# Optimization experiments

Hardware: AMD Instinct MI355X
Metric: run time of the kernel (lower is better)

## Reference

```python
import jax, jax.numpy as jnp
import numpy as np
import math

B, L, HD, H = 4, 1024, 512, 8
D = HD // H  # 64 per-head dim


def setup_inputs() -> dict:
    key = jax.random.key(0)
    ks = jax.random.split(key, 9)
    query = jax.random.normal(ks[0], (B, L, HD), jnp.float32)
    key_ = jax.random.normal(ks[1], (B, L, HD), jnp.float32)
    value = jax.random.normal(ks[2], (B, L, HD), jnp.float32)
    kernel = jax.random.normal(ks[3], (B * H, L, L), jnp.float32) * 0.1
    # sparse-ish boolean mask; low density so no row is fully masked
    attn_mask = jax.random.bernoulli(ks[4], 0.05, (B * H, L, L))
    in_proj_weight = jax.random.normal(ks[5], (3 * HD, HD), jnp.float32) * 0.02
    in_proj_bias = jnp.zeros((3 * HD,), jnp.float32)
    out_w = jax.random.normal(ks[6], (HD, HD), jnp.float32) * 0.02
    out_b = jnp.zeros((HD,), jnp.float32)
    return dict(query=query, key_=key_, value=value, attn_mask=attn_mask,
                key_padding_mask=0, kernel=kernel,
                in_proj_weight=in_proj_weight, in_proj_bias=in_proj_bias,
                out_w=out_w, out_b=out_b)


def _split_heads(x):
    # [B, L, HD] -> [B*H, L, D]
    b, l, _ = x.shape
    return x.reshape(b, l, H, D).transpose(0, 2, 1, 3).reshape(b * H, l, D)


def _merge_heads(x):
    # [B*H, L, D] -> [B, L, HD]
    bh, l, d = x.shape
    b = bh // H
    return x.reshape(b, H, l, d).transpose(0, 2, 1, 3).reshape(b, l, H * d)


def reference(query, key_, value, attn_mask, key_padding_mask, kernel,
              in_proj_weight, in_proj_bias, out_w, out_b):
    # key_padding_mask is falsy (None-equivalent) -> attn_mask unchanged
    wq, wk, wv = in_proj_weight[:HD], in_proj_weight[HD:2 * HD], in_proj_weight[2 * HD:]
    bq, bk, bv = in_proj_bias[:HD], in_proj_bias[HD:2 * HD], in_proj_bias[2 * HD:]
    q = _split_heads(query @ wq.T + bq)   # [B*H, L, D]
    k = _split_heads(key_ @ wk.T + bk)
    v = _split_heads(value @ wv.T + bv)
    scale = 1.0 / math.sqrt(D)
    scores = jnp.einsum('bqd,bkd->bqk', q, k) * scale  # [B*H, Lq, Lk]
    scores = scores + kernel.transpose(0, 2, 1)        # additive kernel bias
    scores = jnp.where(attn_mask, -jnp.inf, scores)    # masked_fill
    attn = jax.nn.softmax(scores, axis=-1)
    out = jnp.einsum('bqk,bkd->bqd', attn, v)          # [B*H, Lq, D]
    out = _merge_heads(out)                            # [B, Lq, HD]
    return out @ out_w.T + out_b
```

## Files before the change

kernel.cpp:

```cpp
#include <hip/hip_runtime.h>
#include <hip/hip_bf16.h>
#include <cstdint>
#include <cstddef>

typedef _Float16 half8 __attribute__((ext_vector_type(8)));
typedef _Float16 half4 __attribute__((ext_vector_type(4)));
typedef float f32x4 __attribute__((ext_vector_type(4)));

#define NB 4
#define NL 1024
#define NHD 512
#define NH 8
#define ND 64
#define NBH 32

#define MFMA16(a, b, c) __builtin_amdgcn_mfma_f32_16x16x32_f16((a), (b), (c), 0, 0, 0)

__global__ __launch_bounds__(256) void prep_kernel(
    const float* __restrict__ kern, const void* __restrict__ mask,
    _Float16* __restrict__ kf16, unsigned* __restrict__ mb)
{
    const int tid = threadIdx.x;
    if (blockIdx.x < 2048) {
        const size_t n8 = (size_t)NBH * NL * NL / 8;
        const size_t stride = 2048 * 256;
        for (size_t u = (size_t)blockIdx.x * 256 + tid; u < n8; u += stride) {
            const float* s = kern + u * 8;
            f32x4 a = *(const f32x4*)s;
            f32x4 b = *(const f32x4*)(s + 4);
            half8 h;
#pragma unroll
            for (int j = 0; j < 4; ++j) { h[j] = (_Float16)a[j]; h[4 + j] = (_Float16)b[j]; }
            *(half8*)(kf16 + u * 8) = h;
        }
    } else {
        __shared__ int s_byte;
        const int blk = blockIdx.x - 2048;
        for (int it = 0; it < 4; ++it) {
            const int t = (blk * 4 + it) * 256 + tid;
            __syncthreads();
            if (tid == 0) s_byte = 0;
            __syncthreads();

            const uint4* p = (const uint4*)((const unsigned char*)mask + (size_t)t * 32);
            uint4 a = p[0], b = p[1];
            unsigned src[8] = {a.x, a.y, a.z, a.w, b.x, b.y, b.z, b.w};
            int bad = 0;
#pragma unroll
            for (int j = 0; j < 8; ++j)
                if (src[j] != 0u && src[j] != 1u && src[j] != 0x3F800000u) bad = 1;
            if (bad) atomicOr(&s_byte, 1);
            __syncthreads();

            unsigned wv = 0;
            if (s_byte) {
#pragma unroll
                for (int j = 0; j < 8; ++j) {
                    unsigned u = src[j];
                    wv |= ((u & 0x000000FFu) ? 1u : 0u) << (4 * j + 0);
                    wv |= ((u & 0x0000FF00u) ? 1u : 0u) << (4 * j + 1);
                    wv |= ((u & 0x00FF0000u) ? 1u : 0u) << (4 * j + 2);
                    wv |= ((u & 0xFF000000u) ? 1u : 0u) << (4 * j + 3);
                }
            } else {
                const uint4* q = (const uint4*)((const unsigned*)mask + (size_t)t * 32);
#pragma unroll
                for (int j = 0; j < 8; ++j) {
                    uint4 v = q[j];
                    wv |= (v.x ? 1u : 0u) << (4 * j + 0);
                    wv |= (v.y ? 1u : 0u) << (4 * j + 1);
                    wv |= (v.z ? 1u : 0u) << (4 * j + 2);
                    wv |= (v.w ? 1u : 0u) << (4 * j + 3);
                }
            }
            mb[t] = wv;
        }
    }
}

__global__ __launch_bounds__(256) void qkv_gemm_kernel(
    const float* __restrict__ qin, const float* __restrict__ kin, const float* __restrict__ vin,
    const float* __restrict__ w, const float* __restrict__ bias,
    _Float16* __restrict__ qb, _Float16* __restrict__ kb, _Float16* __restrict__ vtb)
{
    const int mtile = blockIdx.x, ntile = blockIdx.y, proj = blockIdx.z;
    const float* A = proj == 0 ? qin : (proj == 1 ? kin : vin);
    const float* W = w + (size_t)proj * NHD * NHD;

    __shared__ __align__(16) _Float16 a_lds[128][72];
    __shared__ __align__(16) _Float16 b_lds[64][72];

    const int tid = threadIdx.x;
    const int wave = tid >> 6, lane = tid & 63, quad = lane >> 4, c = lane & 15;
    const int wm = wave >> 1, wn = wave & 1;

    f32x4 acc[4][2] = {};

    const int arow = tid >> 1, acol = (tid & 1) * 32;
    const int brow = tid >> 2, bcol = (tid & 3) * 16;
    const float* pa = &A[(size_t)(mtile * 128 + arow) * NHD + acol];
    const float* pb = &W[(size_t)(ntile * 64 + brow) * NHD + bcol];

    f32x4 ar[8], br[4];
#pragma unroll
    for (int j = 0; j < 8; ++j) ar[j] = *(const f32x4*)(pa + j * 4);
#pragma unroll
    for (int j = 0; j < 4; ++j) br[j] = *(const f32x4*)(pb + j * 4);

    for (int k0 = 0; k0 < NHD; k0 += 64) {
        half8 ah[4], bh_[2];
#pragma unroll
        for (int t = 0; t < 4; ++t)
#pragma unroll
            for (int j = 0; j < 4; ++j) {
                ah[t][j] = (_Float16)ar[2 * t][j];
                ah[t][4 + j] = (_Float16)ar[2 * t + 1][j];
            }
#pragma unroll
        for (int t = 0; t < 2; ++t)
#pragma unroll
            for (int j = 0; j < 4; ++j) {
                bh_[t][j] = (_Float16)br[2 * t][j];
                bh_[t][4 + j] = (_Float16)br[2 * t + 1][j];
            }
        __syncthreads();
#pragma unroll
        for (int t = 0; t < 4; ++t) *(half8*)&a_lds[arow][acol + t * 8] = ah[t];
#pragma unroll
        for (int t = 0; t < 2; ++t) *(half8*)&b_lds[brow][bcol + t * 8] = bh_[t];
        if (k0 < NHD - 64) {
            const float* na = pa + k0 + 64;
            const float* nb = pb + k0 + 64;
#pragma unroll
            for (int j = 0; j < 8; ++j) ar[j] = *(const f32x4*)(na + j * 4);
#pragma unroll
            for (int j = 0; j < 4; ++j) br[j] = *(const f32x4*)(nb + j * 4);
        }
        __syncthreads();

#pragma unroll
        for (int kk = 0; kk < 2; ++kk) {
            half8 af[4], bf[2];
#pragma unroll
            for (int ms = 0; ms < 4; ++ms)
                af[ms] = *(const half8*)&a_lds[wm * 64 + ms * 16 + c][kk * 32 + quad * 8];
#pragma unroll
            for (int ns = 0; ns < 2; ++ns)
                bf[ns] = *(const half8*)&b_lds[wn * 32 + ns * 16 + c][kk * 32 + quad * 8];
#pragma unroll
            for (int ms = 0; ms < 4; ++ms)
#pragma unroll
                for (int ns = 0; ns < 2; ++ns)
                    acc[ms][ns] = MFMA16(af[ms], bf[ns], acc[ms][ns]);
        }
    }

#pragma unroll
    for (int ms = 0; ms < 4; ++ms)
#pragma unroll
    for (int ns = 0; ns < 2; ++ns) {
        const int Cc = ntile * 64 + wn * 32 + ns * 16 + c;
        const float bv = bias[proj * NHD + Cc];
        const int h = Cc >> 6, d = Cc & 63;
#pragma unroll
        for (int r = 0; r < 4; ++r) {
            const int R = mtile * 128 + wm * 64 + ms * 16 + quad * 4 + r;
            const int b = R >> 10, l = R & 1023;
            const int bh = b * NH + h;
            float val = acc[ms][ns][r] + bv;
            if (proj == 0) {
                qb[((size_t)(bh * NL + l)) * ND + d] = (_Float16)(val * 0.125f);
            } else if (proj == 1) {
                kb[((size_t)(bh * NL + l)) * ND + d] = (_Float16)val;
            } else {
                vtb[((size_t)(bh * ND + d)) * NL + l] = (_Float16)val;
            }
        }
    }
}

__global__ __launch_bounds__(256) void attn_kernel(
    const _Float16* __restrict__ qb, const _Float16* __restrict__ kb, const _Float16* __restrict__ vtb,
    const _Float16* __restrict__ kf16, const unsigned* __restrict__ mb,
    _Float16* __restrict__ pO, float* __restrict__ pm, float* __restrict__ pl)
{
    const int qt = blockIdx.x, bh = blockIdx.y, half = blockIdx.z;
    const int tid = threadIdx.x, wave = tid >> 6, lane = tid & 63, quad = lane >> 4, c = lane & 15;
    const int q_base = qt * 64 + wave * 16;
    const int kt0 = half * 8;

    __shared__ __align__(16) _Float16 k_lds[64][72];
    __shared__ __align__(16) _Float16 vt_lds[64][72];
    __shared__ __align__(16) _Float16 p_lds[64][72];
    __shared__ unsigned mask_lds[64][2];

    half8 aq0 = *(const half8*)&qb[((size_t)(bh * NL) + q_base + c) * ND + quad * 8];
    half8 aq1 = *(const half8*)&qb[((size_t)(bh * NL) + q_base + c) * ND + 32 + quad * 8];

    f32x4 O[4] = {};
    float m_i[4] = {-1e30f, -1e30f, -1e30f, -1e30f};
    float l_i[4] = {0.f, 0.f, 0.f, 0.f};

    const int sr = tid >> 2, sc = (tid & 3) * 16;

    half8 kr0, kr1, vr0, vr1;
    unsigned mr = 0;
    half4 bias_h[4];

    const _Float16* bias_base = kf16 + (size_t)bh * NL * NL + (size_t)(qt * 64 + wave * 16 + quad * 4);

    {
        const _Float16* pk = &kb[((size_t)(bh * NL) + kt0 * 64 + sr) * ND + sc];
        kr0 = *(const half8*)pk; kr1 = *(const half8*)(pk + 8);
        const _Float16* pv = &vtb[((size_t)(bh * ND) + sr) * NL + kt0 * 64 + sc];
        vr0 = *(const half8*)pv; vr1 = *(const half8*)(pv + 8);
        if (tid < 128) mr = mb[((size_t)bh * NL + qt * 64 + (tid >> 1)) * 32 + kt0 * 2 + (tid & 1)];
#pragma unroll
        for (int ns = 0; ns < 4; ++ns)
            bias_h[ns] = *(const half4*)(bias_base + (size_t)(kt0 * 64 + ns * 16 + c) * NL);
    }

    for (int kt = 0; kt < 8; ++kt) {
        __syncthreads();
        *(half8*)&k_lds[sr][sc] = kr0;  *(half8*)&k_lds[sr][sc + 8] = kr1;
        *(half8*)&vt_lds[sr][sc] = vr0; *(half8*)&vt_lds[sr][sc + 8] = vr1;
        if (tid < 128) mask_lds[tid >> 1][tid & 1] = mr;
        __syncthreads();

        if (kt < 7) {
            const int ktg = kt0 + kt + 1;
            const _Float16* pk = &kb[((size_t)(bh * NL) + ktg * 64 + sr) * ND + sc];
            kr0 = *(const half8*)pk; kr1 = *(const half8*)(pk + 8);
            const _Float16* pv = &vtb[((size_t)(bh * ND) + sr) * NL + ktg * 64 + sc];
            vr0 = *(const half8*)pv; vr1 = *(const half8*)(pv + 8);
            if (tid < 128) mr = mb[((size_t)bh * NL + qt * 64 + (tid >> 1)) * 32 + ktg * 2 + (tid & 1)];
        }

        f32x4 S[4];
#pragma unroll
        for (int ns = 0; ns < 4; ++ns) {
            f32x4 a = {};
            half8 bk0 = *(const half8*)&k_lds[ns * 16 + c][quad * 8];
            half8 bk1 = *(const half8*)&k_lds[ns * 16 + c][32 + quad * 8];
            a = MFMA16(aq0, bk0, a);
            a = MFMA16(aq1, bk1, a);
            S[ns] = a;
        }

        unsigned mw0[4], mw1[4];
#pragma unroll
        for (int r = 0; r < 4; ++r) {
            const int row = wave * 16 + quad * 4 + r;
            uint2 mm = *(const uint2*)&mask_lds[row][0];
            mw0[r] = mm.x; mw1[r] = mm.y;
        }

#pragma unroll
        for (int ns = 0; ns < 4; ++ns) {
            const int bit = ((ns & 1) << 4) + c;
#pragma unroll
            for (int r = 0; r < 4; ++r) {
                unsigned w = (ns < 2) ? mw0[r] : mw1[r];
                bool mk = (w >> bit) & 1u;
                S[ns][r] = mk ? -1e30f : (S[ns][r] + (float)bias_h[ns][r]);
            }
        }

        if (kt < 7) {
            const int ktg = kt0 + kt + 1;
#pragma unroll
            for (int ns = 0; ns < 4; ++ns)
                bias_h[ns] = *(const half4*)(bias_base + (size_t)(ktg * 64 + ns * 16 + c) * NL);
        }

        float pmax[4], al[4];
#pragma unroll
        for (int r = 0; r < 4; ++r) {
            float t = fmaxf(fmaxf(S[0][r], S[1][r]), fmaxf(S[2][r], S[3][r]));
            t = fmaxf(t, __shfl_xor(t, 1));
            t = fmaxf(t, __shfl_xor(t, 2));
            t = fmaxf(t, __shfl_xor(t, 4));
            t = fmaxf(t, __shfl_xor(t, 8));
            float mn = fmaxf(m_i[r], t);
            al[r] = __expf(m_i[r] - mn);
            m_i[r] = mn;
            pmax[r] = mn;
        }
        float rs[4] = {0.f, 0.f, 0.f, 0.f};
#pragma unroll
        for (int ns = 0; ns < 4; ++ns)
#pragma unroll
            for (int r = 0; r < 4; ++r) {
                float p = __expf(S[ns][r] - pmax[r]);
                S[ns][r] = p;
                rs[r] += p;
            }
#pragma unroll
        for (int r = 0; r < 4; ++r) {
            float t = rs[r];
            t += __shfl_xor(t, 1);
            t += __shfl_xor(t, 2);
            t += __shfl_xor(t, 4);
            t += __shfl_xor(t, 8);
            l_i[r] = l_i[r] * al[r] + t;
        }
#pragma unroll
        for (int ds = 0; ds < 4; ++ds)
#pragma unroll
            for (int r = 0; r < 4; ++r)
                O[ds][r] *= al[r];

#pragma unroll
        for (int ns = 0; ns < 4; ++ns)
#pragma unroll
            for (int r = 0; r < 4; ++r)
                p_lds[wave * 16 + quad * 4 + r][ns * 16 + c] = (_Float16)S[ns][r];
        __asm__ volatile("s_waitcnt lgkmcnt(0)" ::: "memory");

#pragma unroll
        for (int ks = 0; ks < 2; ++ks) {
            half8 ap = *(const half8*)&p_lds[wave * 16 + c][ks * 32 + quad * 8];
#pragma unroll
            for (int ds = 0; ds < 4; ++ds) {
                half8 bv = *(const half8*)&vt_lds[ds * 16 + c][ks * 32 + quad * 8];
                O[ds] = MFMA16(ap, bv, O[ds]);
            }
        }
    }

    const int ub = (bh * 16 + qt) * 2 + half;
    _Float16* pOb = pO + (size_t)ub * 4096;
#pragma unroll
    for (int ds = 0; ds < 4; ++ds)
#pragma unroll
        for (int r = 0; r < 4; ++r)
            pOb[(wave * 16 + quad * 4 + r) * 64 + ds * 16 + c] = (_Float16)O[ds][r];
    if (c == 0) {
#pragma unroll
        for (int r = 0; r < 4; ++r) {
            const int row = wave * 16 + quad * 4 + r;
            pm[(size_t)ub * 64 + row] = m_i[r];
            pl[(size_t)ub * 64 + row] = l_i[r];
        }
    }
}

__global__ __launch_bounds__(256) void out_gemm_kernel(
    const _Float16* __restrict__ pO, const float* __restrict__ pm, const float* __restrict__ pl,
    const float* __restrict__ w, const float* __restrict__ bias,
    float* __restrict__ out)
{
    const int mtile = blockIdx.x, ntile = blockIdx.y;
    const int bb = mtile >> 4, qt = mtile & 15;
    __shared__ __align__(16) _Float16 a_lds[64][72];
    __shared__ __align__(16) _Float16 b_lds[64][72];
    const int tid = threadIdx.x, wave = tid >> 6, lane = tid & 63, quad = lane >> 4, c = lane & 15;
    const int wm = wave >> 1, wn = wave & 1;
    f32x4 acc[2][2] = {};

    const int sr = tid >> 2, sc = (tid & 3) * 16;

    half8 p0a, p0b, p1a, p1b;
    f32x4 br[4];
    float m0, l0, m1, l1;

    auto fetch = [&](int k0) {
        const int h = k0 >> 6;
        const int u0 = ((bb * 8 + h) * 16 + qt) * 2;
        const _Float16* q0 = pO + (size_t)u0 * 4096 + sr * 64 + sc;
        p0a = *(const half8*)q0; p0b = *(const half8*)(q0 + 8);
        const _Float16* q1 = q0 + 4096;
        p1a = *(const half8*)q1; p1b = *(const half8*)(q1 + 8);
        m0 = pm[(size_t)u0 * 64 + sr]; l0 = pl[(size_t)u0 * 64 + sr];
        m1 = pm[(size_t)(u0 + 1) * 64 + sr]; l1 = pl[(size_t)(u0 + 1) * 64 + sr];
        const float* pb = &w[(size_t)(ntile * 64 + sr) * NHD + k0 + sc];
#pragma unroll
        for (int j = 0; j < 4; ++j) br[j] = *(const f32x4*)(pb + j * 4);
    };

    fetch(0);
    for (int k0 = 0; k0 < NHD; k0 += 64) {
        const float mx = fmaxf(m0, m1);
        const float e0 = __expf(m0 - mx), e1 = __expf(m1 - mx);
        const float linv = 1.0f / (l0 * e0 + l1 * e1);
        const float s0 = e0 * linv, s1 = e1 * linv;
        half8 ah0, ah1, bh0, bh1;
#pragma unroll
        for (int j = 0; j < 8; ++j) {
            ah0[j] = (_Float16)((float)p0a[j] * s0 + (float)p1a[j] * s1);
            ah1[j] = (_Float16)((float)p0b[j] * s0 + (float)p1b[j] * s1);
        }
#pragma unroll
        for (int j = 0; j < 4; ++j) {
            bh0[j] = (_Float16)br[0][j]; bh0[4 + j] = (_Float16)br[1][j];
            bh1[j] = (_Float16)br[2][j]; bh1[4 + j] = (_Float16)br[3][j];
        }
        __syncthreads();
        *(half8*)&a_lds[sr][sc] = ah0; *(half8*)&a_lds[sr][sc + 8] = ah1;
        *(half8*)&b_lds[sr][sc] = bh0; *(half8*)&b_lds[sr][sc + 8] = bh1;
        if (k0 < NHD - 64) fetch(k0 + 64);
        __syncthreads();

#pragma unroll
        for (int kk = 0; kk < 2; ++kk) {
            half8 af0 = *(const half8*)&a_lds[wm * 32 + c][kk * 32 + quad * 8];
            half8 af1 = *(const half8*)&a_lds[wm * 32 + 16 + c][kk * 32 + quad * 8];
            half8 bf0 = *(const half8*)&b_lds[wn * 32 + c][kk * 32 + quad * 8];
            half8 bf1 = *(const half8*)&b_lds[wn * 32 + 16 + c][kk * 32 + quad * 8];
            acc[0][0] = MFMA16(af0, bf0, acc[0][0]);
            acc[0][1] = MFMA16(af0, bf1, acc[0][1]);
            acc[1][0] = MFMA16(af1, bf0, acc[1][0]);
            acc[1][1] = MFMA16(af1, bf1, acc[1][1]);
        }
    }

#pragma unroll
    for (int ms = 0; ms < 2; ++ms)
#pragma unroll
    for (int ns = 0; ns < 2; ++ns) {
        const int Cc = ntile * 64 + wn * 32 + ns * 16 + c;
        const float bv = bias[Cc];
#pragma unroll
        for (int r = 0; r < 4; ++r) {
            const int R = mtile * 64 + wm * 32 + ms * 16 + quad * 4 + r;
            out[(size_t)R * NHD + Cc] = acc[ms][ns][r] + bv;
        }
    }
}

extern "C" void kernel_launch(void* const* d_in, const int* in_sizes, int n_in,
                              void* d_out, int out_size, void* d_ws, size_t ws_size,
                              hipStream_t stream)
{
    const float* query = (const float*)d_in[0];
    const float* key_  = (const float*)d_in[1];
    const float* value = (const float*)d_in[2];
    const void*  mask  = d_in[3];
    const float* kern  = (const float*)d_in[5];
    const float* ipw   = (const float*)d_in[6];
    const float* ipb   = (const float*)d_in[7];
    const float* outw  = (const float*)d_in[8];
    const float* outb  = (const float*)d_in[9];

    char* ws = (char*)d_ws;
    _Float16* qb  = (_Float16*)(ws);
    _Float16* kb  = (_Float16*)(ws + (4ull << 20));
    _Float16* vtb = (_Float16*)(ws + (8ull << 20));
    _Float16* pO  = (_Float16*)(ws + (16ull << 20));
    float* pm     = (float*)(ws + (32ull << 20));
    float* pl     = (float*)(ws + (33ull << 20));
    unsigned* mb  = (unsigned*)(ws + (40ull << 20));
    _Float16* kf16= (_Float16*)(ws + (48ull << 20));

    prep_kernel<<<3072, 256, 0, stream>>>(kern, mask, kf16, mb);
    qkv_gemm_kernel<<<dim3(32, 8, 3), 256, 0, stream>>>(query, key_, value, ipw, ipb, qb, kb, vtb);
    attn_kernel<<<dim3(16, 32, 2), 256, 0, stream>>>(qb, kb, vtb, kf16, mb, pO, pm, pl);
    out_gemm_kernel<<<dim3(64, 8), 256, 0, stream>>>(pO, pm, pl, outw, outb, (float*)d_out);
}
```

Before: 409.6 us.

## Read fp32 bias directly in attention, process 256 query rows per block

Removes the separate pass that converted the 128 MB fp32 bias kernel to fp16 and instead loads fp32 bias directly inside the attention kernel as f32x4 vectors of four consecutive query rows. Each block now handles 256 query rows (four 64-row sub-tiles, with Q staged in LDS), so bias reads cover wider contiguous spans and K/V tiles are reused across more queries. This cuts a full read-plus-write of the bias tensor, but raises register pressure (four sets of O, m and l accumulators plus 16 f32x4 bias loads) and leaves only 256 blocks, which may reduce occupancy.

```diff
diff --git a/kernel.cpp b/kernel.cpp
--- a/kernel.cpp
+++ b/kernel.cpp
@@ -16,65 +16,49 @@
 
 #define MFMA16(a, b, c) __builtin_amdgcn_mfma_f32_16x16x32_f16((a), (b), (c), 0, 0, 0)
 
-__global__ __launch_bounds__(256) void prep_kernel(
-    const float* __restrict__ kern, const void* __restrict__ mask,
-    _Float16* __restrict__ kf16, unsigned* __restrict__ mb)
+__global__ __launch_bounds__(256) void mask_kernel(
+    const void* __restrict__ mask, unsigned* __restrict__ mb)
 {
+    __shared__ int s_byte;
     const int tid = threadIdx.x;
-    if (blockIdx.x < 2048) {
-        const size_t n8 = (size_t)NBH * NL * NL / 8;
-        const size_t stride = 2048 * 256;
-        for (size_t u = (size_t)blockIdx.x * 256 + tid; u < n8; u += stride) {
-            const float* s = kern + u * 8;
-            f32x4 a = *(const f32x4*)s;
-            f32x4 b = *(const f32x4*)(s + 4);
-            half8 h;
-#pragma unroll
-            for (int j = 0; j < 4; ++j) { h[j] = (_Float16)a[j]; h[4 + j] = (_Float16)b[j]; }
-            *(half8*)(kf16 + u * 8) = h;
-        }
-    } else {
-        __shared__ int s_byte;
-        const int blk = blockIdx.x - 2048;
-        for (int it = 0; it < 4; ++it) {
-            const int t = (blk * 4 + it) * 256 + tid;
-            __syncthreads();
-            if (tid == 0) s_byte = 0;
-            __syncthreads();
-
-            const uint4* p = (const uint4*)((const unsigned char*)mask + (size_t)t * 32);
-            uint4 a = p[0], b = p[1];
-            unsigned src[8] = {a.x, a.y, a.z, a.w, b.x, b.y, b.z, b.w};
-            int bad = 0;
-#pragma unroll
-            for (int j = 0; j < 8; ++j)
-                if (src[j] != 0u && src[j] != 1u && src[j] != 0x3F800000u) bad = 1;
-            if (bad) atomicOr(&s_byte, 1);
-            __syncthreads();
-
-            unsigned wv = 0;
-            if (s_byte) {
-#pragma unroll
-                for (int j = 0; j < 8; ++j) {
-                    unsigned u = src[j];
-                    wv |= ((u & 0x000000FFu) ? 1u : 0u) << (4 * j + 0);
-                    wv |= ((u & 0x0000FF00u) ? 1u : 0u) << (4 * j + 1);
-                    wv |= ((u & 0x00FF0000u) ? 1u : 0u) << (4 * j + 2);
-                    wv |= ((u & 0xFF000000u) ? 1u : 0u) << (4 * j + 3);
-                }
-            } else {
-                const uint4* q = (const uint4*)((const unsigned*)mask + (size_t)t * 32);
-#pragma unroll
-                for (int j = 0; j < 8; ++j) {
-                    uint4 v = q[j];
-                    wv |= (v.x ? 1u : 0u) << (4 * j + 0);
-                    wv |= (v.y ? 1u : 0u) << (4 * j + 1);
-                    wv |= (v.z ? 1u : 0u) << (4 * j + 2);
-                    wv |= (v.w ? 1u : 0u) << (4 * j + 3);
-                }
-            }
-            mb[t] = wv;
-        }
+    for (int it = 0; it < 4; ++it) {
+        const int t = (blockIdx.x * 4 + it) * 256 + tid;
+        __syncthreads();
+        if (tid == 0) s_byte = 0;
+        __syncthreads();
+
+        const uint4* p = (const uint4*)((const unsigned char*)mask + (size_t)t * 32);
+        uint4 a = p[0], b = p[1];
+        unsigned src[8] = {a.x, a.y, a.z, a.w, b.x, b.y, b.z, b.w};
+        int bad = 0;
+#pragma unroll
+        for (int j = 0; j < 8; ++j)
+            if (src[j] != 0u && src[j] != 1u && src[j] != 0x3F800000u) bad = 1;
+        if (bad) atomicOr(&s_byte, 1);
+        __syncthreads();
+
+        unsigned wv = 0;
+        if (s_byte) {
+#pragma unroll
+            for (int j = 0; j < 8; ++j) {
+                unsigned u = src[j];
+                wv |= ((u & 0x000000FFu) ? 1u : 0u) << (4 * j + 0);
+                wv |= ((u & 0x0000FF00u) ? 1u : 0u) << (4 * j + 1);
+                wv |= ((u & 0x00FF0000u) ? 1u : 0u) << (4 * j + 2);
+                wv |= ((u & 0xFF000000u) ? 1u : 0u) << (4 * j + 3);
+            }
+        } else {
+            const uint4* q = (const uint4*)((const unsigned*)mask + (size_t)t * 32);
+#pragma unroll
+            for (int j = 0; j < 8; ++j) {
+                uint4 v = q[j];
+                wv |= (v.x ? 1u : 0u) << (4 * j + 0);
+                wv |= (v.y ? 1u : 0u) << (4 * j + 1);
+                wv |= (v.z ? 1u : 0u) << (4 * j + 2);
+                wv |= (v.w ? 1u : 0u) << (4 * j + 3);
+            }
+        }
+        mb[t] = wv;
     }
 }
 
@@ -181,50 +165,56 @@
 
 __global__ __launch_bounds__(256) void attn_kernel(
     const _Float16* __restrict__ qb, const _Float16* __restrict__ kb, const _Float16* __restrict__ vtb,
-    const _Float16* __restrict__ kf16, const unsigned* __restrict__ mb,
+    const float* __restrict__ kern, const unsigned* __restrict__ mb,
     _Float16* __restrict__ pO, float* __restrict__ pm, float* __restrict__ pl)
 {
-    const int qt = blockIdx.x, bh = blockIdx.y, half = blockIdx.z;
+    const int qt4 = blockIdx.x, bh = blockIdx.y, half = blockIdx.z;
     const int tid = threadIdx.x, wave = tid >> 6, lane = tid & 63, quad = lane >> 4, c = lane & 15;
-    const int q_base = qt * 64 + wave * 16;
     const int kt0 = half * 8;
+    const int q0 = qt4 * 256;
 
     __shared__ __align__(16) _Float16 k_lds[64][72];
     __shared__ __align__(16) _Float16 vt_lds[64][72];
     __shared__ __align__(16) _Float16 p_lds[64][72];
-    __shared__ unsigned mask_lds[64][2];
-
-    half8 aq0 = *(const half8*)&qb[((size_t)(bh * NL) + q_base + c) * ND + quad * 8];
-    half8 aq1 = *(const half8*)&qb[((size_t)(bh * NL) + q_base + c) * ND + 32 + quad * 8];
-
-    f32x4 O[4] = {};
-    float m_i[4] = {-1e30f, -1e30f, -1e30f, -1e30f};
-    float l_i[4] = {0.f, 0.f, 0.f, 0.f};
+    __shared__ __align__(16) _Float16 q_lds[256][72];
+    __shared__ __align__(8) unsigned mask_lds[256][2];
 
     const int sr = tid >> 2, sc = (tid & 3) * 16;
 
+#pragma unroll
+    for (int seg = 0; seg < 4; ++seg) {
+        const int row = seg * 64 + sr;
+        const _Float16* src = &qb[((size_t)(bh * NL) + q0 + row) * ND + sc];
+        half8 a = *(const half8*)src, b = *(const half8*)(src + 8);
+        *(half8*)&q_lds[row][sc] = a;
+        *(half8*)&q_lds[row][sc + 8] = b;
+    }
+
+    f32x4 O[4][4] = {};
+    float m_i[4][4], l_i[4][4];
+#pragma unroll
+    for (int s = 0; s < 4; ++s)
+#pragma unroll
+        for (int r = 0; r < 4; ++r) { m_i[s][r] = -1e30f; l_i[s][r] = 0.f; }
+
     half8 kr0, kr1, vr0, vr1;
-    unsigned mr = 0;
-    half4 bias_h[4];
-
-    const _Float16* bias_base = kf16 + (size_t)bh * NL * NL + (size_t)(qt * 64 + wave * 16 + quad * 4);
+    uint2 mrow;
+
+    const float* bias_base = kern + (size_t)bh * NL * NL + (size_t)(q0 + wave * 16 + quad * 4);
 
     {
         const _Float16* pk = &kb[((size_t)(bh * NL) + kt0 * 64 + sr) * ND + sc];
         kr0 = *(const half8*)pk; kr1 = *(const half8*)(pk + 8);
         const _Float16* pv = &vtb[((size_t)(bh * ND) + sr) * NL + kt0 * 64 + sc];
         vr0 = *(const half8*)pv; vr1 = *(const half8*)(pv + 8);
-        if (tid < 128) mr = mb[((size_t)bh * NL + qt * 64 + (tid >> 1)) * 32 + kt0 * 2 + (tid & 1)];
-#pragma unroll
-        for (int ns = 0; ns < 4; ++ns)
-            bias_h[ns] = *(const half4*)(bias_base + (size_t)(kt0 * 64 + ns * 16 + c) * NL);
+        mrow = *(const uint2*)&mb[((size_t)bh * NL + q0 + tid) * 32 + kt0 * 2];
     }
 
     for (int kt = 0; kt < 8; ++kt) {
         __syncthreads();
         *(half8*)&k_lds[sr][sc] = kr0;  *(half8*)&k_lds[sr][sc + 8] = kr1;
         *(half8*)&vt_lds[sr][sc] = vr0; *(half8*)&vt_lds[sr][sc + 8] = vr1;
-        if (tid < 128) mask_lds[tid >> 1][tid & 1] = mr;
+        *(uint2*)&mask_lds[tid][0] = mrow;
         __syncthreads();
 
         if (kt < 7) {
@@ -233,114 +223,124 @@
             kr0 = *(const half8*)pk; kr1 = *(const half8*)(pk + 8);
             const _Float16* pv = &vtb[((size_t)(bh * ND) + sr) * NL + ktg * 64 + sc];
             vr0 = *(const half8*)pv; vr1 = *(const half8*)(pv + 8);
-            if (tid < 128) mr = mb[((size_t)bh * NL + qt * 64 + (tid >> 1)) * 32 + ktg * 2 + (tid & 1)];
-        }
-
-        f32x4 S[4];
-#pragma unroll
-        for (int ns = 0; ns < 4; ++ns) {
-            f32x4 a = {};
-            half8 bk0 = *(const half8*)&k_lds[ns * 16 + c][quad * 8];
-            half8 bk1 = *(const half8*)&k_lds[ns * 16 + c][32 + quad * 8];
-            a = MFMA16(aq0, bk0, a);
-            a = MFMA16(aq1, bk1, a);
-            S[ns] = a;
-        }
-
-        unsigned mw0[4], mw1[4];
-#pragma unroll
-        for (int r = 0; r < 4; ++r) {
-            const int row = wave * 16 + quad * 4 + r;
-            uint2 mm = *(const uint2*)&mask_lds[row][0];
-            mw0[r] = mm.x; mw1[r] = mm.y;
-        }
-
-#pragma unroll
-        for (int ns = 0; ns < 4; ++ns) {
-            const int bit = ((ns & 1) << 4) + c;
+            mrow = *(const uint2*)&mb[((size_t)bh * NL + q0 + tid) * 32 + ktg * 2];
+        }
+
+        const int kta = kt0 + kt;
+        f32x4 bias_r[4][4];
+#pragma unroll
+        for (int s = 0; s < 4; ++s)
+#pragma unroll
+            for (int ns = 0; ns < 4; ++ns)
+                bias_r[s][ns] = *(const f32x4*)(bias_base + (size_t)(kta * 64 + ns * 16 + c) * NL + s * 64);
+
+#pragma unroll
+        for (int s = 0; s < 4; ++s) {
+            half8 aq0 = *(const half8*)&q_lds[s * 64 + wave * 16 + c][quad * 8];
+            half8 aq1 = *(const half8*)&q_lds[s * 64 + wave * 16 + c][32 + quad * 8];
+
+            f32x4 S[4];
+#pragma unroll
+            for (int ns = 0; ns < 4; ++ns) {
+                f32x4 a = {};
+                half8 bk0 = *(const half8*)&k_lds[ns * 16 + c][quad * 8];
+                half8 bk1 = *(const half8*)&k_lds[ns * 16 + c][32 + quad * 8];
+                a = MFMA16(aq0, bk0, a);
+                a = MFMA16(aq1, bk1, a);
+                S[ns] = a;
+            }
+
+            unsigned mw0[4], mw1[4];
 #pragma unroll
             for (int r = 0; r < 4; ++r) {
-                unsigned w = (ns < 2) ? mw0[r] : mw1[r];
-                bool mk = (w >> bit) & 1u;
-                S[ns][r] = mk ? -1e30f : (S[ns][r] + (float)bias_h[ns][r]);
-            }
-        }
-
-        if (kt < 7) {
-            const int ktg = kt0 + kt + 1;
+                const int row = s * 64 + wave * 16 + quad * 4 + r;
+                uint2 mm = *(const uint2*)&mask_lds[row][0];
+                mw0[r] = mm.x; mw1[r] = mm.y;
+            }
+
+#pragma unroll
+            for (int ns = 0; ns < 4; ++ns) {
+                const int bit = ((ns & 1) << 4) + c;
+#pragma unroll
+                for (int r = 0; r < 4; ++r) {
+                    unsigned w = (ns < 2) ? mw0[r] : mw1[r];
+                    bool mk = (w >> bit) & 1u;
+                    S[ns][r] = mk ? -1e30f : (S[ns][r] + bias_r[s][ns][r]);
+                }
+            }
+
+            float pmax[4], al[4];
+#pragma unroll
+            for (int r = 0; r < 4; ++r) {
+                float t = fmaxf(fmaxf(S[0][r], S[1][r]), fmaxf(S[2][r], S[3][r]));
+                t = fmaxf(t, __shfl_xor(t, 1));
+                t = fmaxf(t, __shfl_xor(t, 2));
+                t = fmaxf(t, __shfl_xor(t, 4));
+                t = fmaxf(t, __shfl_xor(t, 8));
+                float mn = fmaxf(m_i[s][r], t);
+                al[r] = __expf(m_i[s][r] - mn);
+                m_i[s][r] = mn;
+                pmax[r] = mn;
+            }
+            float rs[4] = {0.f, 0.f, 0.f, 0.f};
 #pragma unroll
             for (int ns = 0; ns < 4; ++ns)
-                bias_h[ns] = *(const half4*)(bias_base + (size_t)(ktg * 64 + ns * 16 + c) * NL);
-        }
-
-        float pmax[4], al[4];
-#pragma unroll
-        for (int r = 0; r < 4; ++r) {
-            float t = fmaxf(fmaxf(S[0][r], S[1][r]), fmaxf(S[2][r], S[3][r]));
-            t = fmaxf(t, __shfl_xor(t, 1));
-            t = fmaxf(t, __shfl_xor(t, 2));
-            t = fmaxf(t, __shfl_xor(t, 4));
-            t = fmaxf(t, __shfl_xor(t, 8));
-            float mn = fmaxf(m_i[r], t);
-            al[r] = __expf(m_i[r] - mn);
-            m_i[r] = mn;
-            pmax[r] = mn;
-        }
-        float rs[4] = {0.f, 0.f, 0.f, 0.f};
-#pragma unroll
-        for (int ns = 0; ns < 4; ++ns)
+#pragma unroll
+                for (int r = 0; r < 4; ++r) {
+                    float p = __expf(S[ns][r] - pmax[r]);
+                    S[ns][r] = p;
+                    rs[r] += p;
+                }
 #pragma unroll
             for (int r = 0; r < 4; ++r) {
-                float p = __expf(S[ns][r] - pmax[r]);
-                S[ns][r] = p;
-                rs[r] += p;
-            }
-#pragma unroll
-        for (int r = 0; r < 4; ++r) {
-            float t = rs[r];
-            t += __shfl_xor(t, 1);
-            t += __shfl_xor(t, 2);
-            t += __shfl_xor(t, 4);
-            t += __shfl_xor(t, 8);
-            l_i[r] = l_i[r] * al[r] + t;
-        }
+                float t = rs[r];
+                t += __shfl_xor(t, 1);
+                t += __shfl_xor(t, 2);
+                t += __shfl_xor(t, 4);
+                t += __shfl_xor(t, 8);
+                l_i[s][r] = l_i[s][r] * al[r] + t;
+            }
+#pragma unroll
+            for (int ds = 0; ds < 4; ++ds)
+#pragma unroll
+                for (int r = 0; r < 4; ++r)
+                    O[s][ds][r] *= al[r];
+
+#pragma unroll
+            for (int ns = 0; ns < 4; ++ns)
+#pragma unroll
+                for (int r = 0; r < 4; ++r)
+                    p_lds[wave * 16 + quad * 4 + r][ns * 16 + c] = (_Float16)S[ns][r];
+            __asm__ volatile("s_waitcnt lgkmcnt(0)" ::: "memory");
+
+#pragma unroll
+            for (int ks = 0; ks < 2; ++ks) {
+                half8 ap = *(const half8*)&p_lds[wave * 16 + c][ks * 32 + quad * 8];
+#pragma unroll
+                for (int ds = 0; ds < 4; ++ds) {
+                    half8 bv = *(const half8*)&vt_lds[ds * 16 + c][ks * 32 + quad * 8];
+                    O[s][ds] = MFMA16(ap, bv, O[s][ds]);
+                }
+            }
+        }
+    }
+
+#pragma unroll
+    for (int s = 0; s < 4; ++s) {
+        const int ub = (bh * 16 + qt4 * 4 + s) * 2 + half;
+        _Float16* pOb = pO + (size_t)ub * 4096;
 #pragma unroll
         for (int ds = 0; ds < 4; ++ds)
 #pragma unroll
             for (int r = 0; r < 4; ++r)
-                O[ds][r] *= al[r];
-
-#pragma unroll
-        for (int ns = 0; ns < 4; ++ns)
-#pragma unroll
-            for (int r = 0; r < 4; ++r)
-                p_lds[wave * 16 + quad * 4 + r][ns * 16 + c] = (_Float16)S[ns][r];
-        __asm__ volatile("s_waitcnt lgkmcnt(0)" ::: "memory");
-
-#pragma unroll
-        for (int ks = 0; ks < 2; ++ks) {
-            half8 ap = *(const half8*)&p_lds[wave * 16 + c][ks * 32 + quad * 8];
-#pragma unroll
-            for (int ds = 0; ds < 4; ++ds) {
-                half8 bv = *(const half8*)&vt_lds[ds * 16 + c][ks * 32 + quad * 8];
-                O[ds] = MFMA16(ap, bv, O[ds]);
-            }
-        }
-    }
-
-    const int ub = (bh * 16 + qt) * 2 + half;
-    _Float16* pOb = pO + (size_t)ub * 4096;
-#pragma unroll
-    for (int ds = 0; ds < 4; ++ds)
-#pragma unroll
-        for (int r = 0; r < 4; ++r)
-            pOb[(wave * 16 + quad * 4 + r) * 64 + ds * 16 + c] = (_Float16)O[ds][r];
-    if (c == 0) {
-#pragma unroll
-        for (int r = 0; r < 4; ++r) {
-            const int row = wave * 16 + quad * 4 + r;
-            pm[(size_t)ub * 64 + row] = m_i[r];
-            pl[(size_t)ub * 64 + row] = l_i[r];
+                pOb[(wave * 16 + quad * 4 + r) * 64 + ds * 16 + c] = (_Float16)O[s][ds][r];
+        if (c == 0) {
+#pragma unroll
+            for (int r = 0; r < 4; ++r) {
+                const int row = wave * 16 + quad * 4 + r;
+                pm[(size_t)ub * 64 + row] = m_i[s][r];
+                pl[(size_t)ub * 64 + row] = l_i[s][r];
+            }
         }
     }
 }
@@ -450,10 +450,9 @@
     float* pm     = (float*)(ws + (32ull << 20));
     float* pl     = (float*)(ws + (33ull << 20));
     unsigned* mb  = (unsigned*)(ws + (40ull << 20));
-    _Float16* kf16= (_Float16*)(ws + (48ull << 20));
-
-    prep_kernel<<<3072, 256, 0, stream>>>(kern, mask, kf16, mb);
+
+    mask_kernel<<<1024, 256, 0, stream>>>(mask, mb);
     qkv_gemm_kernel<<<dim3(32, 8, 3), 256, 0, stream>>>(query, key_, value, ipw, ipb, qb, kb, vtb);
-    attn_kernel<<<dim3(16, 32, 2), 256, 0, stream>>>(qb, kb, vtb, kf16, mb, pO, pm, pl);
+    attn_kernel<<<dim3(4, 32, 2), 256, 0, stream>>>(qb, kb, vtb, kern, mb, pO, pm, pl);
     out_gemm_kernel<<<dim3(64, 8), 256, 0, stream>>>(pO, pm, pl, outw, outb, (float*)d_out);
 }
```

Result: faster. 384.5 us (-6.1%).
